# Performance work log

Hardware: AMD Instinct MI355X
Metric: run time of the kernel (lower is better)

## Reference

```python
import jax, jax.numpy as jnp
import numpy as np

KSIZE = 7
PAD = KSIZE // 2          # reflection pad radius
EPS_BN = 1e-5             # CONFIG.model.arch.batchnorm_eps
SCALE = 1.0               # self.scale
BN_W, BN_B = 0.1, 0.0     # BatchNorm init per module


def _l2n(x, eps=1e-12):
    return x / (jnp.linalg.norm(x) + eps)


def setup_inputs() -> dict:
    key = jax.random.key(0)
    ks = jax.random.split(key, 6)
    B, Cg, Co, H, W = 2, 128, 32, 512, 512
    f = jax.random.normal(ks[0], (B, Cg, H, W), jnp.float32)
    alpha = jax.random.normal(ks[1], (B, Co, H, W), jnp.float32)
    # guidance_conv: 1x1 conv Cg -> Cg//2 (xavier-ish init)
    wg = jax.random.normal(ks[2], (Cg // 2, Cg), jnp.float32) * (1.0 / np.sqrt(Cg))
    bg = jnp.zeros((Cg // 2,), jnp.float32)
    # spectral-norm 1x1 conv Co -> Co, no bias
    w_bar = jax.random.normal(ks[3], (Co, Co), jnp.float32) * (1.0 / np.sqrt(Co))
    u = _l2n(jax.random.normal(ks[4], (Co,), jnp.float32))
    v = _l2n(jax.random.normal(ks[5], (Co,), jnp.float32))
    return {"f": f, "alpha": alpha, "wg": wg, "bg": bg, "w_bar": w_bar, "u": u, "v": v}


def reference(f, alpha, wg, bg, w_bar, u, v):
    B, _, H, W = f.shape
    # 1x1 guidance conv
    g = jnp.einsum('oc,bchw->bohw', wg, f) + bg[None, :, None, None]
    # hop_normalize: channel-wise L2 normalize, clamped at 1e-4
    gn = g / jnp.maximum(jnp.linalg.norm(g, axis=1, keepdims=True), 1e-4)
    r = jnp.pad(gn, ((0, 0), (0, 0), (PAD, PAD), (PAD, PAD)), mode='reflect')
    # ksize^2 shifted-window correlation -> scores [K2, B, 1, H, W]
    scores = []
    for i in range(KSIZE):
        for j in range(KSIZE):
            if i == PAD and j == PAD:
                scores.append(jnp.full((B, 1, H, W), -10000.0, gn.dtype))
            else:
                scores.append((gn * r[:, :, i:i + H, j:j + W]).sum(axis=1, keepdims=True))
    s = jax.nn.softmax(jnp.stack(scores, axis=0) * SCALE, axis=0)
    # weighted neighborhood aggregation of alpha (skip center tap)
    alp = jnp.pad(alpha, ((0, 0), (0, 0), (PAD, PAD), (PAD, PAD)), mode='reflect')
    y = jnp.zeros_like(alpha)
    for i in range(KSIZE):
        for j in range(KSIZE):
            if i == PAD and j == PAD:
                continue
            y = y + alp[:, :, i:i + H, j:j + W] * s[i * KSIZE + j]
    # spectral-norm 1x1 conv (training: one detached power iteration)
    v1 = jax.lax.stop_gradient(_l2n(w_bar.T @ u))
    u1 = jax.lax.stop_gradient(_l2n(w_bar @ v1))
    sigma = u1 @ (w_bar @ v1)
    w_sn = w_bar / sigma
    y2 = jnp.einsum('oc,bchw->bohw', w_sn, y)
    # BatchNorm2d, training mode (batch stats), weight=0.1 bias=0
    mean = y2.mean(axis=(0, 2, 3), keepdims=True)
    var = y2.var(axis=(0, 2, 3), keepdims=True)
    y_bn = BN_W * (y2 - mean) / jnp.sqrt(var + EPS_BN) + BN_B
    return y_bn + alpha
```

## Files before the change

kernel.cpp:

```cpp
#include <hip/hip_runtime.h>

#define HWc   262144
#define CGc   128
#define CHc   64
#define COc   32
#define NPIXc 524288
#define TW 32
#define TH 8
#define HLW 38
#define HLH 14
#define HPX (HLW*HLH)

typedef _Float16 h2    __attribute__((ext_vector_type(2)));
typedef __fp16   fp2   __attribute__((ext_vector_type(2)));
typedef _Float16 f16x8 __attribute__((ext_vector_type(8)));
typedef float    f32x4 __attribute__((ext_vector_type(4)));

union AB { uint4 q; f16x8 v; h2 p[4]; unsigned u[4]; };

__device__ __forceinline__ int refl(int p){
  if (p < 0) p = -p;
  else if (p >= 512) p = 1022 - p;
  return p;
}
__device__ __forceinline__ h2 as_h2(unsigned u){ union{unsigned u; h2 h;} x; x.u = u; return x.h; }
__device__ __forceinline__ unsigned as_u(h2 h){ union{unsigned u; h2 h;} x; x.h = h; return x.u; }
__device__ __forceinline__ unsigned pkh(float a, float b){
  h2 h; h.x = (_Float16)a; h.y = (_Float16)b; return as_u(h);
}
__device__ __forceinline__ h2 pkrtz(float a, float b){
  union{ fp2 f; h2 h; } x; x.f = __builtin_amdgcn_cvt_pkrtz(a, b); return x.h;
}
__device__ __forceinline__ float2 upk(unsigned u){
  h2 h = as_h2(u); return make_float2((float)h.x, (float)h.y);
}
__device__ __forceinline__ float dot2h(unsigned a, unsigned b, float c){
  return __builtin_amdgcn_fdot2(as_h2(a), as_h2(b), c, false);
}
__device__ __forceinline__ void mixlo(float& acc, unsigned ab, float e){
  asm("v_fma_mix_f32 %0, %1, %2, %0 op_sel:[0,0,0] op_sel_hi:[1,0,0]"
      : "+v"(acc) : "v"(ab), "v"(e));
}
__device__ __forceinline__ void mixhi(float& acc, unsigned ab, float e){
  asm("v_fma_mix_f32 %0, %1, %2, %0 op_sel:[1,0,0] op_sel_hi:[1,0,0]"
      : "+v"(acc) : "v"(ab), "v"(e));
}

__global__ void k0_prep(const float* __restrict__ wbar, const float* __restrict__ u,
                        const float* __restrict__ wg,
                        unsigned* __restrict__ wgA, unsigned* __restrict__ wsnA){
  const int t = threadIdx.x;
  __shared__ float sv1[32];
  float tv = 0.f;
  if (t < 32){
    #pragma unroll
    for (int o = 0; o < 32; o++) tv += wbar[o*32 + t] * u[o];
  }
  float sq = tv * tv;
  #pragma unroll
  for (int off = 32; off; off >>= 1) sq += __shfl_down(sq, off);
  const float n1 = sqrtf(__shfl(sq, 0)) + 1e-12f;
  if (t < 32) sv1[t] = tv / n1;
  __syncthreads();
  float tu = 0.f;
  if (t < 32){
    #pragma unroll
    for (int c = 0; c < 32; c++) tu += wbar[t*32 + c] * sv1[c];
  }
  float sq2 = tu * tu;
  #pragma unroll
  for (int off = 32; off; off >>= 1) sq2 += __shfl_down(sq2, off);
  const float S = __shfl(sq2, 0);
  const float inv = (sqrtf(S) + 1e-12f) / S;

  for (int k = t; k < 4096; k += 64){
    const int mk = k >> 8, L = (k >> 2) & 63, j = k & 3;
    const int m = mk >> 2, ks = mk & 3;
    const int o = m*16 + (L & 15);
    const int c = ks*32 + 8*(L >> 4) + 2*j;
    wgA[k] = pkh(wg[o*128 + c], wg[o*128 + c + 1]);
  }
  for (int k = t; k < 512; k += 64){
    const int m = k >> 8, L = (k >> 2) & 63, j = k & 3;
    const int o = m*16 + (L & 15);
    const int c = 8*(L >> 4) + 2*j;
    wsnA[k] = pkh(wbar[o*32 + c] * inv, wbar[o*32 + c + 1] * inv);
  }
}

__global__ __launch_bounds__(256) void k1m(const float* __restrict__ f,
                                           const float* __restrict__ alpha,
                                           const uint4* __restrict__ wgA,
                                           const uint4* __restrict__ wsnA,
                                           const float* __restrict__ bg,
                                           unsigned* __restrict__ gn,
                                           unsigned* __restrict__ apm){
  const int tid  = threadIdx.x;
  const int lane = tid & 63, w = tid >> 6;
  const int lo   = lane & 15, hi = lane >> 4;

  AB wga[4][4];
  #pragma unroll
  for (int m = 0; m < 4; m++)
    #pragma unroll
    for (int ks = 0; ks < 4; ks++)
      wga[m][ks].q = wgA[(m*4 + ks)*64 + lane];
  AB wsa[2];
  #pragma unroll
  for (int m = 0; m < 2; m++) wsa[m].q = wsnA[m*64 + lane];
  float4 bgl[4];
  #pragma unroll
  for (int m = 0; m < 4; m++) bgl[m] = *(const float4*)(bg + m*16 + hi*4);

  const int pxg = blockIdx.x * 256 + w * 64;

  #pragma unroll 1
  for (int nt = 0; nt < 4; nt++){
    const int px0  = pxg + nt*16;
    const int b    = px0 >> 18;
    const int pix0 = px0 & (HWc - 1);
    const float* fb = f + (size_t)b * CGc * HWc + pix0 + lo;
    const float* ac = alpha + (size_t)b * COc * HWc + pix0 + lo + (size_t)(hi*8) * HWc;

    float fv[32], av[8];
    #pragma unroll
    for (int ks = 0; ks < 4; ks++){
      const float* fc = fb + (size_t)(ks*32 + hi*8) * HWc;
      #pragma unroll
      for (int e = 0; e < 8; e++)
        fv[ks*8 + e] = fc[(size_t)e * HWc];
    }
    #pragma unroll
    for (int e = 0; e < 8; e++)
      av[e] = ac[(size_t)e * HWc];

    f32x4 acc[4];
    #pragma unroll
    for (int m = 0; m < 4; m++) acc[m] = (f32x4){0.f, 0.f, 0.f, 0.f};

    #pragma unroll
    for (int ks = 0; ks < 4; ks++){
      AB bf;
      #pragma unroll
      for (int j = 0; j < 4; j++)
        bf.p[j] = pkrtz(fv[ks*8 + 2*j], fv[ks*8 + 2*j + 1]);
      #pragma unroll
      for (int m = 0; m < 4; m++)
        acc[m] = __builtin_amdgcn_mfma_f32_16x16x32_f16(wga[m][ks].v, bf.v, acc[m], 0, 0, 0);
    }

    float v[16]; float nsq = 0.f;
    #pragma unroll
    for (int m = 0; m < 4; m++){
      v[4*m+0] = acc[m][0] + bgl[m].x;
      v[4*m+1] = acc[m][1] + bgl[m].y;
      v[4*m+2] = acc[m][2] + bgl[m].z;
      v[4*m+3] = acc[m][3] + bgl[m].w;
      nsq = fmaf(v[4*m+0], v[4*m+0], nsq); nsq = fmaf(v[4*m+1], v[4*m+1], nsq);
      nsq = fmaf(v[4*m+2], v[4*m+2], nsq); nsq = fmaf(v[4*m+3], v[4*m+3], nsq);
    }
    nsq += __shfl_xor(nsq, 16);
    nsq += __shfl_xor(nsq, 32);
    const float inv = 1.f / fmaxf(sqrtf(nsq), 1e-4f);

    unsigned* gp = gn + (size_t)(px0 + lo) * 32 + hi*2;
    #pragma unroll
    for (int m = 0; m < 4; m++){
      uint2 st = make_uint2(pkh(v[4*m+0]*inv, v[4*m+1]*inv),
                            pkh(v[4*m+2]*inv, v[4*m+3]*inv));
      *(uint2*)(gp + m*8) = st;
    }

    AB af;
    #pragma unroll
    for (int j = 0; j < 4; j++)
      af.p[j] = pkrtz(av[2*j], av[2*j + 1]);
    unsigned* op = apm + (size_t)(px0 + lo) * 16 + hi*2;
    #pragma unroll
    for (int m = 0; m < 2; m++){
      f32x4 aa = (f32x4){0.f, 0.f, 0.f, 0.f};
      aa = __builtin_amdgcn_mfma_f32_16x16x32_f16(wsa[m].v, af.v, aa, 0, 0, 0);
      uint2 st = make_uint2(pkh(aa[0], aa[1]), pkh(aa[2], aa[3]));
      *(uint2*)(op + m*8) = st;
    }
  }
}

__global__ __launch_bounds__(256) void k2_agg(const unsigned* __restrict__ gn,
                                              const unsigned* __restrict__ apm,
                                              unsigned* __restrict__ y2){
  __shared__ uint4 gs4[8][HPX];

  const int lb  = (blockIdx.x & 7) * 256 + (blockIdx.x >> 3);
  const int txx = lb & 15;
  const int tyy = (lb >> 4) & 63;
  const int bb  = lb >> 10;
  const int x0  = txx * TW, y0 = tyy * TH;
  const int tid = threadIdx.x;

  for (int t = tid; t < HPX; t += 256){
    const int hr = t / HLW;
    const int hc = t - hr * HLW;
    const int gy = refl(y0 + hr - 3);
    const int gx = refl(x0 + hc - 3);
    const uint4* src = (const uint4*)(gn + (size_t)((bb << 18) + (gy << 9) + gx) * 32);
    #pragma unroll
    for (int k = 0; k < 8; k++) gs4[k][t] = src[k];
  }
  __syncthreads();

  const int r  = tid >> 5, c = tid & 31;
  const int yy = y0 + r,  xx = x0 + c;
  const int self = (r + 3) * HLW + (c + 3);

  uint4 cv[8];
  #pragma unroll
  for (int k = 0; k < 8; k++) cv[k] = gs4[k][self];

  int ax[7];
  #pragma unroll
  for (int j = 0; j < 7; j++) ax[j] = refl(xx + j - 3);

  float yac[COc];
  #pragma unroll
  for (int k = 0; k < COc; k++) yac[k] = 0.f;
  float esum = 0.f;

  #pragma unroll 1
  for (int i = 0; i < 7; i++){
    const int ay = refl(yy + i - 3);
    const unsigned* aprow = apm + (size_t)((bb << 18) + (ay << 9)) * 16;
    const int rowbase = (r + i) * HLW + c;
    #pragma unroll
    for (int j = 0; j < 7; j++){
      if (i == 3 && j == 3) continue;
      const int hp = rowbase + j;
      float s0 = 0.f, s1 = 0.f, s2 = 0.f, s3 = 0.f;
      #pragma unroll
      for (int k = 0; k < 8; k++){
        const uint4 q = gs4[k][hp];
        s0 = dot2h(cv[k].x, q.x, s0);
        s1 = dot2h(cv[k].y, q.y, s1);
        s2 = dot2h(cv[k].z, q.z, s2);
        s3 = dot2h(cv[k].w, q.w, s3);
      }
      const float e = __expf((s0 + s1) + (s2 + s3));
      esum += e;
      const uint4* ap = (const uint4*)(aprow + (size_t)ax[j] * 16);
      #pragma unroll
      for (int kk = 0; kk < 4; kk++){
        const uint4 a = ap[kk];
        mixlo(yac[8*kk+0], a.x, e); mixhi(yac[8*kk+1], a.x, e);
        mixlo(yac[8*kk+2], a.y, e); mixhi(yac[8*kk+3], a.y, e);
        mixlo(yac[8*kk+4], a.z, e); mixhi(yac[8*kk+5], a.z, e);
        mixlo(yac[8*kk+6], a.w, e); mixhi(yac[8*kk+7], a.w, e);
      }
    }
  }

  const float inv = 1.f / esum;
  unsigned yw[16];
  #pragma unroll
  for (int k = 0; k < 16; k++) yw[k] = pkh(yac[2*k] * inv, yac[2*k+1] * inv);
  uint4* yp = (uint4*)(y2 + (size_t)((bb << 18) + (yy << 9) + xx) * 16);
  #pragma unroll
  for (int k = 0; k < 4; k++)
    yp[k] = make_uint4(yw[4*k], yw[4*k+1], yw[4*k+2], yw[4*k+3]);
}

__global__ __launch_bounds__(256) void k3_stats(const unsigned* __restrict__ y2,
                                                float* __restrict__ stats){
  float s[COc], q[COc];
  #pragma unroll
  for (int o = 0; o < COc; o++){ s[o] = 0.f; q[o] = 0.f; }
  const int stride = gridDim.x * 256;
  for (int p = blockIdx.x * 256 + threadIdx.x; p < NPIXc; p += stride){
    const uint4* yp = (const uint4*)(y2 + (size_t)p * 16);
    #pragma unroll
    for (int k = 0; k < 4; k++){
      const uint4 w = yp[k];
      const unsigned vv[4] = {w.x, w.y, w.z, w.w};
      #pragma unroll
      for (int m = 0; m < 4; m++){
        const float2 ab = upk(vv[m]);
        s[8*k+2*m]   += ab.x; q[8*k+2*m]   = fmaf(ab.x, ab.x, q[8*k+2*m]);
        s[8*k+2*m+1] += ab.y; q[8*k+2*m+1] = fmaf(ab.y, ab.y, q[8*k+2*m+1]);
      }
    }
  }
  #pragma unroll
  for (int o = 0; o < COc; o++){
    #pragma unroll
    for (int off = 32; off; off >>= 1){
      s[o] += __shfl_down(s[o], off);
      q[o] += __shfl_down(q[o], off);
    }
  }
  __shared__ float red[4][64];
  const int wv = threadIdx.x >> 6;
  if ((threadIdx.x & 63) == 0){
    #pragma unroll
    for (int o = 0; o < COc; o++){ red[wv][o] = s[o]; red[wv][32 + o] = q[o]; }
  }
  __syncthreads();
  if (threadIdx.x < 64){
    const float v = red[0][threadIdx.x] + red[1][threadIdx.x]
                  + red[2][threadIdx.x] + red[3][threadIdx.x];
    atomicAdd(&stats[threadIdx.x], v);
  }
}

__global__ void k3b_final(const float* __restrict__ stats, float* __restrict__ stats2){
  const int t = threadIdx.x;
  if (t < COc){
    const float invN = 1.f / (float)NPIXc;
    const float mean = stats[t] * invN;
    const float var  = fmaf(-mean, mean, stats[COc + t] * invN);
    stats2[t]       = mean;
    stats2[COc + t] = 0.1f * rsqrtf(var + 1e-5f);
  }
}

__global__ __launch_bounds__(256) void k4_out(const unsigned* __restrict__ y2,
                                              const float* __restrict__ alpha,
                                              const float* __restrict__ stats2,
                                              float* __restrict__ out){
  const int p   = blockIdx.x * 256 + threadIdx.x;
  const int b   = p >> 18;
  const int pix = p & (HWc - 1);
  const uint4* yp = (const uint4*)(y2 + (size_t)p * 16);
  const size_t boff = (size_t)b * COc * HWc + pix;
  #pragma unroll
  for (int k = 0; k < 4; k++){
    const uint4 w = yp[k];
    const unsigned vv[4] = {w.x, w.y, w.z, w.w};
    #pragma unroll
    for (int m = 0; m < 4; m++){
      const int o = 8*k + 2*m;
      const float2 ab = upk(vv[m]);
      out[boff + (size_t)o*HWc]     = fmaf(ab.x - stats2[o],   stats2[COc+o],
                                           alpha[boff + (size_t)o*HWc]);
      out[boff + (size_t)(o+1)*HWc] = fmaf(ab.y - stats2[o+1], stats2[COc+o+1],
                                           alpha[boff + (size_t)(o+1)*HWc]);
    }
  }
}

extern "C" void kernel_launch(void* const* d_in, const int* in_sizes, int n_in,
                              void* d_out, int out_size, void* d_ws, size_t ws_size,
                              hipStream_t stream){
  const float* f     = (const float*)d_in[0];
  const float* alpha = (const float*)d_in[1];
  const float* wg    = (const float*)d_in[2];
  const float* bg    = (const float*)d_in[3];
  const float* wbar  = (const float*)d_in[4];
  const float* u     = (const float*)d_in[5];
  (void)in_sizes; (void)n_in; (void)out_size; (void)ws_size;
  float* out = (float*)d_out;

  char* ws = (char*)d_ws;
  float*    stats  = (float*)ws;
  float*    stats2 = (float*)(ws + 4096);
  unsigned* wgA    = (unsigned*)(ws + 8192);
  unsigned* wsnA   = (unsigned*)(ws + 32768);
  unsigned* apm    = (unsigned*)(ws + 65536);
  unsigned* gn     = (unsigned*)(ws + 65536 + (size_t)NPIXc*64);
  unsigned* y2     = (unsigned*)(ws + 65536 + (size_t)NPIXc*64 + (size_t)NPIXc*128);

  (void)hipMemsetAsync(stats, 0, 64 * sizeof(float), stream);
  k0_prep  <<<1, 64, 0, stream>>>(wbar, u, wg, wgA, wsnA);
  k1m      <<<NPIXc / 256, 256, 0, stream>>>(f, alpha, (const uint4*)wgA,
                                             (const uint4*)wsnA, bg, gn, apm);
  k2_agg   <<<2048, 256, 0, stream>>>(gn, apm, y2);
  k3_stats <<<256, 256, 0, stream>>>(y2, stats);
  k3b_final<<<1, 64, 0, stream>>>(stats, stats2);
  k4_out   <<<NPIXc / 256, 256, 0, stream>>>(y2, alpha, stats2, out);
}
```

Measured before the change: 318.5 us.

## Compute neighborhood scores and aggregation with MFMA instead of per-pixel dot2

Recasts the 7x7 correlation as banded matrix products: each wavefront computes scores for 16 pixels against a 32-wide row window with MFMA, masks out-of-window and center taps, then aggregates alpha with a second MFMA over exponentiated weights. To feed this, the projected alpha buffer switches from pixel-major to channel-planar fp16 so row segments can be loaded as vectors. The MFMAs replace scalar dot2 and fma_mix loops, at the cost of wasted lanes in the banded tiles and fp16 rounding of the softmax weights.

```diff
diff --git a/kernel.cpp b/kernel.cpp
--- a/kernel.cpp
+++ b/kernel.cpp
@@ -10,13 +10,16 @@
 #define HLW 38
 #define HLH 14
 #define HPX (HLW*HLH)
+#define HPAD 545
 
 typedef _Float16 h2    __attribute__((ext_vector_type(2)));
 typedef __fp16   fp2   __attribute__((ext_vector_type(2)));
+typedef _Float16 f16x4 __attribute__((ext_vector_type(4)));
 typedef _Float16 f16x8 __attribute__((ext_vector_type(8)));
 typedef float    f32x4 __attribute__((ext_vector_type(4)));
 
-union AB { uint4 q; f16x8 v; h2 p[4]; unsigned u[4]; };
+union AB  { uint4 q; f16x8 v; h2 p[4]; unsigned u[4]; };
+union AB4 { uint2 q; f16x4 v; h2 p[2]; unsigned u[2]; };
 
 __device__ __forceinline__ int refl(int p){
   if (p < 0) p = -p;
@@ -34,16 +37,11 @@
 __device__ __forceinline__ float2 upk(unsigned u){
   h2 h = as_h2(u); return make_float2((float)h.x, (float)h.y);
 }
-__device__ __forceinline__ float dot2h(unsigned a, unsigned b, float c){
-  return __builtin_amdgcn_fdot2(as_h2(a), as_h2(b), c, false);
-}
-__device__ __forceinline__ void mixlo(float& acc, unsigned ab, float e){
-  asm("v_fma_mix_f32 %0, %1, %2, %0 op_sel:[0,0,0] op_sel_hi:[1,0,0]"
-      : "+v"(acc) : "v"(ab), "v"(e));
-}
-__device__ __forceinline__ void mixhi(float& acc, unsigned ab, float e){
-  asm("v_fma_mix_f32 %0, %1, %2, %0 op_sel:[1,0,0] op_sel_hi:[1,0,0]"
-      : "+v"(acc) : "v"(ab), "v"(e));
+__device__ __forceinline__ f32x4 mfma32(f16x8 a, f16x8 b, f32x4 c){
+  return __builtin_amdgcn_mfma_f32_16x16x32_f16(a, b, c, 0, 0, 0);
+}
+__device__ __forceinline__ f32x4 mfma16(f16x4 a, f16x4 b, f32x4 c){
+  return __builtin_amdgcn_mfma_f32_16x16x16f16(a, b, c, 0, 0, 0);
 }
 
 __global__ void k0_prep(const float* __restrict__ wbar, const float* __restrict__ u,
@@ -94,7 +92,7 @@
                                            const uint4* __restrict__ wsnA,
                                            const float* __restrict__ bg,
                                            unsigned* __restrict__ gn,
-                                           unsigned* __restrict__ apm){
+                                           _Float16* __restrict__ aph){
   const int tid  = threadIdx.x;
   const int lane = tid & 63, w = tid >> 6;
   const int lo   = lane & 15, hi = lane >> 4;
@@ -146,7 +144,7 @@
         bf.p[j] = pkrtz(fv[ks*8 + 2*j], fv[ks*8 + 2*j + 1]);
       #pragma unroll
       for (int m = 0; m < 4; m++)
-        acc[m] = __builtin_amdgcn_mfma_f32_16x16x32_f16(wga[m][ks].v, bf.v, acc[m], 0, 0, 0);
+        acc[m] = mfma32(wga[m][ks].v, bf.v, acc[m]);
     }
 
     float v[16]; float nsq = 0.f;
@@ -175,21 +173,21 @@
     #pragma unroll
     for (int j = 0; j < 4; j++)
       af.p[j] = pkrtz(av[2*j], av[2*j + 1]);
-    unsigned* op = apm + (size_t)(px0 + lo) * 16 + hi*2;
     #pragma unroll
     for (int m = 0; m < 2; m++){
       f32x4 aa = (f32x4){0.f, 0.f, 0.f, 0.f};
-      aa = __builtin_amdgcn_mfma_f32_16x16x32_f16(wsa[m].v, af.v, aa, 0, 0, 0);
-      uint2 st = make_uint2(pkh(aa[0], aa[1]), pkh(aa[2], aa[3]));
-      *(uint2*)(op + m*8) = st;
+      aa = mfma32(wsa[m].v, af.v, aa);
+      #pragma unroll
+      for (int r = 0; r < 4; r++)
+        aph[((size_t)((b << 5) + m*16 + hi*4 + r) << 18) + pix0 + lo] = (_Float16)aa[r];
     }
   }
 }
 
 __global__ __launch_bounds__(256) void k2_agg(const unsigned* __restrict__ gn,
-                                              const unsigned* __restrict__ apm,
+                                              const _Float16* __restrict__ aph,
                                               unsigned* __restrict__ y2){
-  __shared__ uint4 gs4[8][HPX];
+  __shared__ uint4 gs4[8][HPAD];
 
   const int lb  = (blockIdx.x & 7) * 256 + (blockIdx.x >> 3);
   const int txx = lb & 15;
@@ -209,63 +207,91 @@
   }
   __syncthreads();
 
-  const int r  = tid >> 5, c = tid & 31;
-  const int yy = y0 + r,  xx = x0 + c;
-  const int self = (r + 3) * HLW + (c + 3);
-
-  uint4 cv[8];
-  #pragma unroll
-  for (int k = 0; k < 8; k++) cv[k] = gs4[k][self];
-
-  int ax[7];
-  #pragma unroll
-  for (int j = 0; j < 7; j++) ax[j] = refl(xx + j - 3);
-
-  float yac[COc];
-  #pragma unroll
-  for (int k = 0; k < COc; k++) yac[k] = 0.f;
-  float esum = 0.f;
+  const int lane = tid & 63, w = tid >> 6;
+  const int lo   = lane & 15, hi = lane >> 4;
+  const bool interior = (txx != 0) && (txx != 15);
 
   #pragma unroll 1
-  for (int i = 0; i < 7; i++){
-    const int ay = refl(yy + i - 3);
-    const unsigned* aprow = apm + (size_t)((bb << 18) + (ay << 9)) * 16;
-    const int rowbase = (r + i) * HLW + c;
-    #pragma unroll
-    for (int j = 0; j < 7; j++){
-      if (i == 3 && j == 3) continue;
-      const int hp = rowbase + j;
-      float s0 = 0.f, s1 = 0.f, s2 = 0.f, s3 = 0.f;
-      #pragma unroll
-      for (int k = 0; k < 8; k++){
-        const uint4 q = gs4[k][hp];
-        s0 = dot2h(cv[k].x, q.x, s0);
-        s1 = dot2h(cv[k].y, q.y, s1);
-        s2 = dot2h(cv[k].z, q.z, s2);
-        s3 = dot2h(cv[k].w, q.w, s3);
+  for (int q = 0; q < 4; q++){
+    const int sid = w*4 + q;
+    const int rs  = sid >> 1;
+    const int cs  = (sid & 1) * 16;
+
+    const int self = (rs + 3)*HLW + cs + 3 + lo;
+    AB bc0, bc1;
+    bc0.q = gs4[hi][self];
+    bc1.q = gs4[4 + hi][self];
+
+    f32x4 pv0 = (f32x4){0.f,0.f,0.f,0.f}, pv1 = (f32x4){0.f,0.f,0.f,0.f};
+    float esp = 0.f;
+
+    #pragma unroll 1
+    for (int i = 0; i < 7; i++){
+      const int rowb = (rs + i)*HLW + cs - 1;
+
+      int ia0 = rowb + lo;       ia0 = ia0 < 0 ? 0 : (ia0 > HPAD-1 ? HPAD-1 : ia0);
+      int ia1 = rowb + 16 + lo;  ia1 = ia1 < 0 ? 0 : (ia1 > HPAD-1 ? HPAD-1 : ia1);
+      AB an00, an01, an10, an11;
+      an00.q = gs4[hi][ia0]; an01.q = gs4[4 + hi][ia0];
+      an10.q = gs4[hi][ia1]; an11.q = gs4[4 + hi][ia1];
+
+      f32x4 s0 = mfma32(an00.v, bc0.v, (f32x4){0.f,0.f,0.f,0.f});
+      s0 = mfma32(an01.v, bc1.v, s0);
+      f32x4 s1 = mfma32(an10.v, bc0.v, (f32x4){0.f,0.f,0.f,0.f});
+      s1 = mfma32(an11.v, bc1.v, s1);
+
+      const int gy = refl(y0 + rs + i - 3);
+      AB4 pa00, pa01, pa10, pa11;
+      {
+        const size_t r0 = ((size_t)((bb << 5) + lo)      << 18) + (gy << 9);
+        const size_t r1 = ((size_t)((bb << 5) + 16 + lo) << 18) + (gy << 9);
+        const int c0 = x0 + cs - 4 + 4*hi;
+        if (interior){
+          pa00.v = *(const f16x4*)(aph + r0 + c0);
+          pa01.v = *(const f16x4*)(aph + r0 + c0 + 16);
+          pa10.v = *(const f16x4*)(aph + r1 + c0);
+          pa11.v = *(const f16x4*)(aph + r1 + c0 + 16);
+        } else {
+          #pragma unroll
+          for (int e = 0; e < 4; e++){
+            const int ca = refl(c0 + e), cb = refl(c0 + 16 + e);
+            pa00.v[e] = aph[r0 + ca]; pa01.v[e] = aph[r0 + cb];
+            pa10.v[e] = aph[r1 + ca]; pa11.v[e] = aph[r1 + cb];
+          }
+        }
       }
-      const float e = __expf((s0 + s1) + (s2 + s3));
-      esum += e;
-      const uint4* ap = (const uint4*)(aprow + (size_t)ax[j] * 16);
-      #pragma unroll
-      for (int kk = 0; kk < 4; kk++){
-        const uint4 a = ap[kk];
-        mixlo(yac[8*kk+0], a.x, e); mixhi(yac[8*kk+1], a.x, e);
-        mixlo(yac[8*kk+2], a.y, e); mixhi(yac[8*kk+3], a.y, e);
-        mixlo(yac[8*kk+4], a.z, e); mixhi(yac[8*kk+5], a.z, e);
-        mixlo(yac[8*kk+6], a.w, e); mixhi(yac[8*kk+7], a.w, e);
+
+      float e0[4], e1[4];
+      #pragma unroll
+      for (int r = 0; r < 4; r++){
+        const int n0 = 4*hi + r, n1 = 16 + 4*hi + r;
+        const int j0 = n0 - lo - 1, j1 = n1 - lo - 1;
+        const bool v0 = (j0 >= 0) && (j0 <= 6) && !(i == 3 && j0 == 3);
+        const bool v1 = (j1 >= 0) && (j1 <= 6) && !(i == 3 && j1 == 3);
+        e0[r] = v0 ? __expf(s0[r]) : 0.f;
+        e1[r] = v1 ? __expf(s1[r]) : 0.f;
+        esp += e0[r] + e1[r];
       }
-    }
-  }
-
-  const float inv = 1.f / esum;
-  unsigned yw[16];
-  #pragma unroll
-  for (int k = 0; k < 16; k++) yw[k] = pkh(yac[2*k] * inv, yac[2*k+1] * inv);
-  uint4* yp = (uint4*)(y2 + (size_t)((bb << 18) + (yy << 9) + xx) * 16);
-  #pragma unroll
-  for (int k = 0; k < 4; k++)
-    yp[k] = make_uint4(yw[4*k], yw[4*k+1], yw[4*k+2], yw[4*k+3]);
+      AB4 eb0, eb1;
+      eb0.p[0] = pkrtz(e0[0], e0[1]); eb0.p[1] = pkrtz(e0[2], e0[3]);
+      eb1.p[0] = pkrtz(e1[0], e1[1]); eb1.p[1] = pkrtz(e1[2], e1[3]);
+
+      pv0 = mfma16(pa00.v, eb0.v, pv0);
+      pv0 = mfma16(pa01.v, eb1.v, pv0);
+      pv1 = mfma16(pa10.v, eb0.v, pv1);
+      pv1 = mfma16(pa11.v, eb1.v, pv1);
+    }
+
+    esp += __shfl_xor(esp, 16);
+    esp += __shfl_xor(esp, 32);
+    const float inv = 1.f / esp;
+
+    const size_t px = (size_t)((bb << 18) + ((y0 + rs) << 9) + x0 + cs + lo);
+    uint2 st0 = make_uint2(pkh(pv0[0]*inv, pv0[1]*inv), pkh(pv0[2]*inv, pv0[3]*inv));
+    uint2 st1 = make_uint2(pkh(pv1[0]*inv, pv1[1]*inv), pkh(pv1[2]*inv, pv1[3]*inv));
+    *(uint2*)(y2 + px*16 + 2*hi)     = st0;
+    *(uint2*)(y2 + px*16 + 8 + 2*hi) = st1;
+  }
 }
 
 __global__ __launch_bounds__(256) void k3_stats(const unsigned* __restrict__ y2,
@@ -359,19 +385,19 @@
   float* out = (float*)d_out;
 
   char* ws = (char*)d_ws;
-  float*    stats  = (float*)ws;
-  float*    stats2 = (float*)(ws + 4096);
-  unsigned* wgA    = (unsigned*)(ws + 8192);
-  unsigned* wsnA   = (unsigned*)(ws + 32768);
-  unsigned* apm    = (unsigned*)(ws + 65536);
-  unsigned* gn     = (unsigned*)(ws + 65536 + (size_t)NPIXc*64);
-  unsigned* y2     = (unsigned*)(ws + 65536 + (size_t)NPIXc*64 + (size_t)NPIXc*128);
+  float*     stats  = (float*)ws;
+  float*     stats2 = (float*)(ws + 4096);
+  unsigned*  wgA    = (unsigned*)(ws + 8192);
+  unsigned*  wsnA   = (unsigned*)(ws + 32768);
+  _Float16*  aph    = (_Float16*)(ws + 65536);
+  unsigned*  gn     = (unsigned*)(ws + 65536 + (size_t)NPIXc*64);
+  unsigned*  y2     = (unsigned*)(ws + 65536 + (size_t)NPIXc*64 + (size_t)NPIXc*128);
 
   (void)hipMemsetAsync(stats, 0, 64 * sizeof(float), stream);
   k0_prep  <<<1, 64, 0, stream>>>(wbar, u, wg, wgA, wsnA);
   k1m      <<<NPIXc / 256, 256, 0, stream>>>(f, alpha, (const uint4*)wgA,
-                                             (const uint4*)wsnA, bg, gn, apm);
-  k2_agg   <<<2048, 256, 0, stream>>>(gn, apm, y2);
+                                             (const uint4*)wsnA, bg, gn, aph);
+  k2_agg   <<<2048, 256, 0, stream>>>(gn, aph, y2);
   k3_stats <<<256, 256, 0, stream>>>(y2, stats);
   k3b_final<<<1, 64, 0, stream>>>(stats, stats2);
   k4_out   <<<NPIXc / 256, 256, 0, stream>>>(y2, alpha, stats2, out);
```

Result: slower. 460.4 us (+44.6%).
